# Performance work log

Measured on AMD Instinct MI355X. Metric: run time of the kernel, lower is better.

The kernel has to match this reference:

```python
import jax, jax.numpy as jnp
import numpy as np

N_EMBD = 384
HEAD_SIZE = 64
B, T = 512, 256


def setup_inputs() -> dict:
    key = jax.random.key(0)
    ks = jax.random.split(key, 7)
    s = 1.0 / np.sqrt(N_EMBD)  # torch Linear default init scale
    return {
        "x": jax.random.normal(ks[0], (B, T, N_EMBD), dtype=jnp.float32),
        "Wq": jax.random.uniform(ks[1], (N_EMBD, HEAD_SIZE), jnp.float32, -s, s),
        "bq": jax.random.uniform(ks[2], (HEAD_SIZE,), jnp.float32, -s, s),
        "Wk": jax.random.uniform(ks[3], (N_EMBD, HEAD_SIZE), jnp.float32, -s, s),
        "bk": jax.random.uniform(ks[4], (HEAD_SIZE,), jnp.float32, -s, s),
        "Wv": jax.random.uniform(ks[5], (N_EMBD, HEAD_SIZE), jnp.float32, -s, s),
        "bv": jax.random.uniform(ks[6], (HEAD_SIZE,), jnp.float32, -s, s),
    }


def reference(x, Wq, bq, Wk, bk, Wv, bv):
    # Single causal self-attention head (nanoGPT 'Head', eval mode: dropout = identity)
    q = x @ Wq + bq  # [B, T, H]
    k = x @ Wk + bk
    v = x @ Wv + bv
    Tq = x.shape[1]
    scale = x.shape[-1] ** -0.5  # NOTE: source scales by n_embd (C), not head_size
    wei = jnp.einsum("btd,bsd->bts", q, k) * scale  # [B, T, T]
    mask = jnp.tril(jnp.ones((Tq, Tq), dtype=bool))
    wei = jnp.where(mask, wei, -jnp.inf)
    wei = jax.nn.softmax(wei, axis=-1)
    return jnp.einsum("bts,bsd->btd", wei, v)  # [B, T, H]
```

## Files before the change

### kernel.cpp

```cpp
#include <hip/hip_runtime.h>
#include <hip/hip_bf16.h>


#define Bsz 512
#define Tt  256
#define Cc  384
#define Hh  64

typedef __attribute__((ext_vector_type(8))) short bf16x8;
typedef __attribute__((ext_vector_type(4))) float f32x4;

__device__ __forceinline__ unsigned short f2bf(float f) {
    unsigned int u = __float_as_uint(f);
    unsigned int r = (u + 0x7fffu + ((u >> 16) & 1u)) >> 16;
    return (unsigned short)r;
}
__device__ __forceinline__ float bf2f(unsigned short b) {
    return __uint_as_float(((unsigned int)b) << 16);
}
__device__ __forceinline__ bf16x8 pack8(float4 a, float4 b) {
    bf16x8 r;
    r[0] = (short)f2bf(a.x); r[1] = (short)f2bf(a.y);
    r[2] = (short)f2bf(a.z); r[3] = (short)f2bf(a.w);
    r[4] = (short)f2bf(b.x); r[5] = (short)f2bf(b.y);
    r[6] = (short)f2bf(b.z); r[7] = (short)f2bf(b.w);
    return r;
}

__global__ __launch_bounds__(256) void prep_kernel(const float* __restrict__ Wq,
                                                   const float* __restrict__ Wk,
                                                   const float* __restrict__ Wv,
                                                   unsigned short* __restrict__ wt) {
    int idx = blockIdx.x * 256 + threadIdx.x;
    if (idx >= 192 * 384) return;
    int n = idx / 384, k = idx - n * 384;
    const float* W = (n < 64) ? Wq : ((n < 128) ? Wk : Wv);
    wt[n * 384 + k] = f2bf(W[k * 64 + (n & 63)]);
}

__global__ __launch_bounds__(256, 2) void qkv_kernel(const float* __restrict__ x,
                                                     const float* __restrict__ bq,
                                                     const float* __restrict__ bk,
                                                     const float* __restrict__ bv,
                                                     const unsigned short* __restrict__ wt,
                                                     unsigned short* __restrict__ qws,
                                                     unsigned short* __restrict__ kws,
                                                     unsigned short* __restrict__ vws) {
    const int w = threadIdx.x >> 6;
    const int lane = threadIdx.x & 63;
    const int quad = lane >> 4;
    const int cl = lane & 15;
    const int rb = blockIdx.x * 128 + w * 32;

    f32x4 acc[2][12];
    for (int rt = 0; rt < 2; ++rt)
        for (int nt = 0; nt < 12; ++nt) acc[rt][nt] = (f32x4){0.f, 0.f, 0.f, 0.f};

    const float* xr0 = x + (size_t)(rb + cl) * Cc;
    const float* xr1 = x + (size_t)(rb + 16 + cl) * Cc;
    const unsigned short* wrow = wt + (size_t)cl * Cc + quad * 8;

    for (int ks = 0; ks < 12; ++ks) {
        const int k0 = ks * 32 + quad * 8;
        float4 xa = *(const float4*)(xr0 + k0);
        float4 xb = *(const float4*)(xr0 + k0 + 4);
        float4 xc = *(const float4*)(xr1 + k0);
        float4 xd = *(const float4*)(xr1 + k0 + 4);
        bf16x8 a0 = pack8(xa, xb);
        bf16x8 a1 = pack8(xc, xd);
#pragma unroll
        for (int nt = 0; nt < 12; ++nt) {
            bf16x8 bfr = *(const bf16x8*)(wrow + (size_t)nt * 16 * Cc + ks * 32);
            acc[0][nt] = __builtin_amdgcn_mfma_f32_16x16x32_bf16(a0, bfr, acc[0][nt], 0, 0, 0);
            acc[1][nt] = __builtin_amdgcn_mfma_f32_16x16x32_bf16(a1, bfr, acc[1][nt], 0, 0, 0);
        }
    }

    for (int nt = 0; nt < 12; ++nt) {
        int col = nt * 16 + cl;
        float bias = (col < 64) ? bq[col] : ((col < 128) ? bk[col - 64] : bv[col - 128]);
        unsigned short* wsout = (col < 64) ? qws : ((col < 128) ? kws : vws);
        int h = col & 63;
        for (int rt = 0; rt < 2; ++rt)
            for (int r = 0; r < 4; ++r) {
                int m = rb + rt * 16 + quad * 4 + r;
                wsout[(size_t)m * Hh + h] = f2bf(acc[rt][nt][r] + bias);
            }
    }
}

__global__ __launch_bounds__(256) void attn_kernel(const unsigned short* __restrict__ qws,
                                                   const unsigned short* __restrict__ kws,
                                                   const unsigned short* __restrict__ vws,
                                                   float* __restrict__ out) {
    __shared__ unsigned short Kl[128 * 72];
    __shared__ unsigned short Vt[64 * 136];
    __shared__ unsigned short Ql[64 * 72];
    __shared__ unsigned short Pl[4 * 16 * 136];

    const int w = threadIdx.x >> 6;
    const int lane = threadIdx.x & 63;
    const int quad = lane >> 4;
    const int cl = lane & 15;
    const int qbase = blockIdx.x * 64;
    const int bb = blockIdx.y;
    const int qrow0 = qbase + w * 16;
    const float SL2E = 0.07362224f;

    for (int l = threadIdx.x; l < 512; l += 256) {
        int row = l >> 3, off = (l & 7) << 3;
        uint4 v = *(const uint4*)(qws + ((size_t)(bb * Tt + qbase + row)) * Hh + off);
        *(uint4*)&Ql[row * 72 + off] = v;
    }

    f32x4 o[4];
    for (int ht = 0; ht < 4; ++ht) o[ht] = (f32x4){0.f, 0.f, 0.f, 0.f};
    float rs[4] = {0.f, 0.f, 0.f, 0.f};

    const int nchunk = (qbase + 191) >> 7;
    for (int c = 0; c < nchunk; ++c) {
        const int kbase = c * 128;
        for (int l = threadIdx.x; l < 1024; l += 256) {
            int row = l >> 3, off = (l & 7) << 3;
            uint4 v = *(const uint4*)(kws + ((size_t)(bb * Tt + kbase + row)) * Hh + off);
            *(uint4*)&Kl[row * 72 + off] = v;
        }
        for (int l = threadIdx.x; l < 1024; l += 256) {
            int s = l >> 3, h0 = (l & 7) << 3;
            uint4 v = *(const uint4*)(vws + ((size_t)(bb * Tt + kbase + s)) * Hh + h0);
            const unsigned short* e = (const unsigned short*)&v;
            for (int j = 0; j < 8; ++j) Vt[(h0 + j) * 136 + s] = e[j];
        }
        __syncthreads();

        bf16x8 aq0 = *(const bf16x8*)&Ql[(w * 16 + cl) * 72 + quad * 8];
        bf16x8 aq1 = *(const bf16x8*)&Ql[(w * 16 + cl) * 72 + 32 + quad * 8];

        const int qlast = qrow0 + 15;
        const int kt = min(8, ((qlast - kbase) >> 4) + 1);
        const int ktr = (kt + 1) & ~1;

        for (int ct = 0; ct < kt; ++ct) {
            f32x4 sc = (f32x4){0.f, 0.f, 0.f, 0.f};
            bf16x8 b0 = *(const bf16x8*)&Kl[(ct * 16 + cl) * 72 + quad * 8];
            bf16x8 b1 = *(const bf16x8*)&Kl[(ct * 16 + cl) * 72 + 32 + quad * 8];
            sc = __builtin_amdgcn_mfma_f32_16x16x32_bf16(aq0, b0, sc, 0, 0, 0);
            sc = __builtin_amdgcn_mfma_f32_16x16x32_bf16(aq1, b1, sc, 0, 0, 0);
            int key = kbase + ct * 16 + cl;
            for (int r = 0; r < 4; ++r) {
                int qg = qrow0 + quad * 4 + r;
                float p = 0.f;
                if (key <= qg) p = exp2f(sc[r] * SL2E);
                unsigned short pb = f2bf(p);
                rs[r] += bf2f(pb);
                Pl[(w * 16 + quad * 4 + r) * 136 + ct * 16 + cl] = pb;
            }
        }
        for (int ct = kt; ct < ktr; ++ct)
            for (int r = 0; r < 4; ++r)
                Pl[(w * 16 + quad * 4 + r) * 136 + ct * 16 + cl] = 0;

        asm volatile("s_waitcnt lgkmcnt(0)" ::: "memory");

        for (int ks2 = 0; ks2 < (ktr >> 1); ++ks2) {
            bf16x8 ap = *(const bf16x8*)&Pl[(w * 16 + cl) * 136 + ks2 * 32 + quad * 8];
            for (int ht = 0; ht < 4; ++ht) {
                bf16x8 bvf = *(const bf16x8*)&Vt[(ht * 16 + cl) * 136 + ks2 * 32 + quad * 8];
                o[ht] = __builtin_amdgcn_mfma_f32_16x16x32_bf16(ap, bvf, o[ht], 0, 0, 0);
            }
        }
        if (c + 1 < nchunk) __syncthreads();
    }

    for (int r = 0; r < 4; ++r) {
        float s = rs[r];
        s += __shfl_xor(s, 1);
        s += __shfl_xor(s, 2);
        s += __shfl_xor(s, 4);
        s += __shfl_xor(s, 8);
        float inv = 1.0f / s;
        int t = qrow0 + quad * 4 + r;
        for (int ht = 0; ht < 4; ++ht)
            out[((size_t)(bb * Tt + t)) * Hh + ht * 16 + cl] = o[ht][r] * inv;
    }
}

extern "C" void kernel_launch(void* const* d_in, const int* in_sizes, int n_in,
                              void* d_out, int out_size, void* d_ws, size_t ws_size,
                              hipStream_t stream) {
    const float* x  = (const float*)d_in[0];
    const float* Wq = (const float*)d_in[1];
    const float* bq = (const float*)d_in[2];
    const float* Wk = (const float*)d_in[3];
    const float* bk = (const float*)d_in[4];
    const float* Wv = (const float*)d_in[5];
    const float* bv = (const float*)d_in[6];
    float* out = (float*)d_out;

    char* ws = (char*)d_ws;
    unsigned short* wt  = (unsigned short*)(ws);
    unsigned short* qws = (unsigned short*)(ws + (size_t)(1  << 20));
    unsigned short* kws = (unsigned short*)(ws + (size_t)(17 << 20));
    unsigned short* vws = (unsigned short*)(ws + (size_t)(33 << 20));

    prep_kernel<<<288, 256, 0, stream>>>(Wq, Wk, Wv, wt);
    qkv_kernel<<<1024, 256, 0, stream>>>(x, bq, bk, bv, wt, qws, kws, vws);
    attn_kernel<<<dim3(4, Bsz), 256, 0, stream>>>(qws, kws, vws, out);
}
```

Measured before the change: 388.4 us.

## Split QKV GEMM across waves, prefetch operands, store V transposed globally

The QKV projection kernel now gives each wave 32 rows by 96 columns instead of 32 by 192, uses twice as many blocks, and raises the occupancy hint. It also software-prefetches the next k-step of x and weights into registers. V is written to global memory already transposed as [B,H,T] with packed 64-bit stores, so the attention kernel loads V into LDS with vector copies instead of a scalar transpose scatter. Other changes are a packed bf16 conversion helper and added unroll pragmas. The cost is more redundant reads of x across column groups and strided transposed global writes for V.

```diff
diff --git a/kernel.cpp b/kernel.cpp
--- a/kernel.cpp
+++ b/kernel.cpp
@@ -19,12 +19,12 @@
     return __uint_as_float(((unsigned int)b) << 16);
 }
 __device__ __forceinline__ bf16x8 pack8(float4 a, float4 b) {
-    bf16x8 r;
-    r[0] = (short)f2bf(a.x); r[1] = (short)f2bf(a.y);
-    r[2] = (short)f2bf(a.z); r[3] = (short)f2bf(a.w);
-    r[4] = (short)f2bf(b.x); r[5] = (short)f2bf(b.y);
-    r[6] = (short)f2bf(b.z); r[7] = (short)f2bf(b.w);
-    return r;
+    union { __hip_bfloat162 h2[4]; bf16x8 v; } u;
+    u.h2[0] = __float22bfloat162_rn(float2{a.x, a.y});
+    u.h2[1] = __float22bfloat162_rn(float2{a.z, a.w});
+    u.h2[2] = __float22bfloat162_rn(float2{b.x, b.y});
+    u.h2[3] = __float22bfloat162_rn(float2{b.z, b.w});
+    return u.v;
 }
 
 __global__ __launch_bounds__(256) void prep_kernel(const float* __restrict__ Wq,
@@ -38,60 +38,103 @@
     wt[n * 384 + k] = f2bf(W[k * 64 + (n & 63)]);
 }
 
-__global__ __launch_bounds__(256, 2) void qkv_kernel(const float* __restrict__ x,
+__global__ __launch_bounds__(256, 4) void qkv_kernel(const float* __restrict__ x,
                                                      const float* __restrict__ bq,
                                                      const float* __restrict__ bk,
                                                      const float* __restrict__ bv,
                                                      const unsigned short* __restrict__ wt,
                                                      unsigned short* __restrict__ qws,
                                                      unsigned short* __restrict__ kws,
-                                                     unsigned short* __restrict__ vws) {
+                                                     unsigned short* __restrict__ vtg) {
     const int w = threadIdx.x >> 6;
     const int lane = threadIdx.x & 63;
     const int quad = lane >> 4;
     const int cl = lane & 15;
-    const int rb = blockIdx.x * 128 + w * 32;
-
-    f32x4 acc[2][12];
+    const int rg = w >> 1, cg = w & 1;
+    const int rw = blockIdx.x * 64 + rg * 32;
+
+    f32x4 acc[2][6];
+#pragma unroll
     for (int rt = 0; rt < 2; ++rt)
-        for (int nt = 0; nt < 12; ++nt) acc[rt][nt] = (f32x4){0.f, 0.f, 0.f, 0.f};
-
-    const float* xr0 = x + (size_t)(rb + cl) * Cc;
-    const float* xr1 = x + (size_t)(rb + 16 + cl) * Cc;
-    const unsigned short* wrow = wt + (size_t)cl * Cc + quad * 8;
-
+#pragma unroll
+        for (int nt = 0; nt < 6; ++nt) acc[rt][nt] = (f32x4){0.f, 0.f, 0.f, 0.f};
+
+    const float* xr0 = x + (size_t)(rw + cl) * Cc + quad * 8;
+    const float* xr1 = x + (size_t)(rw + 16 + cl) * Cc + quad * 8;
+    const unsigned short* wrow = wt + ((size_t)(cg * 96) + cl) * Cc + quad * 8;
+
+    float4 cx[4];
+    bf16x8 cb[6];
+    cx[0] = *(const float4*)(xr0);
+    cx[1] = *(const float4*)(xr0 + 4);
+    cx[2] = *(const float4*)(xr1);
+    cx[3] = *(const float4*)(xr1 + 4);
+#pragma unroll
+    for (int nt = 0; nt < 6; ++nt) cb[nt] = *(const bf16x8*)(wrow + (size_t)nt * 16 * Cc);
+
+#pragma unroll
     for (int ks = 0; ks < 12; ++ks) {
-        const int k0 = ks * 32 + quad * 8;
-        float4 xa = *(const float4*)(xr0 + k0);
-        float4 xb = *(const float4*)(xr0 + k0 + 4);
-        float4 xc = *(const float4*)(xr1 + k0);
-        float4 xd = *(const float4*)(xr1 + k0 + 4);
-        bf16x8 a0 = pack8(xa, xb);
-        bf16x8 a1 = pack8(xc, xd);
-#pragma unroll
-        for (int nt = 0; nt < 12; ++nt) {
-            bf16x8 bfr = *(const bf16x8*)(wrow + (size_t)nt * 16 * Cc + ks * 32);
-            acc[0][nt] = __builtin_amdgcn_mfma_f32_16x16x32_bf16(a0, bfr, acc[0][nt], 0, 0, 0);
-            acc[1][nt] = __builtin_amdgcn_mfma_f32_16x16x32_bf16(a1, bfr, acc[1][nt], 0, 0, 0);
-        }
-    }
-
-    for (int nt = 0; nt < 12; ++nt) {
-        int col = nt * 16 + cl;
-        float bias = (col < 64) ? bq[col] : ((col < 128) ? bk[col - 64] : bv[col - 128]);
-        unsigned short* wsout = (col < 64) ? qws : ((col < 128) ? kws : vws);
-        int h = col & 63;
-        for (int rt = 0; rt < 2; ++rt)
-            for (int r = 0; r < 4; ++r) {
-                int m = rb + rt * 16 + quad * 4 + r;
-                wsout[(size_t)m * Hh + h] = f2bf(acc[rt][nt][r] + bias);
+        float4 nx[4];
+        bf16x8 nb[6];
+        if (ks + 1 < 12) {
+            const int k1 = (ks + 1) * 32;
+            nx[0] = *(const float4*)(xr0 + k1);
+            nx[1] = *(const float4*)(xr0 + k1 + 4);
+            nx[2] = *(const float4*)(xr1 + k1);
+            nx[3] = *(const float4*)(xr1 + k1 + 4);
+#pragma unroll
+            for (int nt = 0; nt < 6; ++nt)
+                nb[nt] = *(const bf16x8*)(wrow + (size_t)nt * 16 * Cc + k1);
+        }
+        bf16x8 a0 = pack8(cx[0], cx[1]);
+        bf16x8 a1 = pack8(cx[2], cx[3]);
+#pragma unroll
+        for (int nt = 0; nt < 6; ++nt) {
+            acc[0][nt] = __builtin_amdgcn_mfma_f32_16x16x32_bf16(a0, cb[nt], acc[0][nt], 0, 0, 0);
+            acc[1][nt] = __builtin_amdgcn_mfma_f32_16x16x32_bf16(a1, cb[nt], acc[1][nt], 0, 0, 0);
+        }
+        if (ks + 1 < 12) {
+#pragma unroll
+            for (int i = 0; i < 4; ++i) cx[i] = nx[i];
+#pragma unroll
+            for (int nt = 0; nt < 6; ++nt) cb[nt] = nb[nt];
+        }
+    }
+
+#pragma unroll
+    for (int nt = 0; nt < 6; ++nt) {
+        int col = cg * 96 + nt * 16 + cl;
+        if (col < 128) {
+            float bias = (col < 64) ? bq[col] : bk[col - 64];
+            unsigned short* o = (col < 64) ? qws : kws;
+            int h = col & 63;
+#pragma unroll
+            for (int rt = 0; rt < 2; ++rt)
+#pragma unroll
+                for (int r = 0; r < 4; ++r) {
+                    int m = rw + rt * 16 + quad * 4 + r;
+                    o[(size_t)m * Hh + h] = f2bf(acc[rt][nt][r] + bias);
+                }
+        } else {
+            int h = col - 128;
+            float bias = bv[h];
+#pragma unroll
+            for (int rt = 0; rt < 2; ++rt) {
+                int m0 = rw + rt * 16 + quad * 4;
+                unsigned long long pk =
+                      (unsigned long long)f2bf(acc[rt][nt][0] + bias)
+                    | ((unsigned long long)f2bf(acc[rt][nt][1] + bias) << 16)
+                    | ((unsigned long long)f2bf(acc[rt][nt][2] + bias) << 32)
+                    | ((unsigned long long)f2bf(acc[rt][nt][3] + bias) << 48);
+                *(unsigned long long*)&vtg[((size_t)(m0 >> 8) * Hh + h) * Tt + (m0 & 255)] = pk;
             }
+        }
     }
 }
 
 __global__ __launch_bounds__(256) void attn_kernel(const unsigned short* __restrict__ qws,
                                                    const unsigned short* __restrict__ kws,
-                                                   const unsigned short* __restrict__ vws,
+                                                   const unsigned short* __restrict__ vtg,
                                                    float* __restrict__ out) {
     __shared__ unsigned short Kl[128 * 72];
     __shared__ unsigned short Vt[64 * 136];
@@ -114,6 +157,7 @@
     }
 
     f32x4 o[4];
+#pragma unroll
     for (int ht = 0; ht < 4; ++ht) o[ht] = (f32x4){0.f, 0.f, 0.f, 0.f};
     float rs[4] = {0.f, 0.f, 0.f, 0.f};
 
@@ -126,10 +170,9 @@
             *(uint4*)&Kl[row * 72 + off] = v;
         }
         for (int l = threadIdx.x; l < 1024; l += 256) {
-            int s = l >> 3, h0 = (l & 7) << 3;
-            uint4 v = *(const uint4*)(vws + ((size_t)(bb * Tt + kbase + s)) * Hh + h0);
-            const unsigned short* e = (const unsigned short*)&v;
-            for (int j = 0; j < 8; ++j) Vt[(h0 + j) * 136 + s] = e[j];
+            int h = l >> 4, off = (l & 15) << 3;
+            uint4 v = *(const uint4*)(vtg + ((size_t)(bb * Hh + h)) * Tt + kbase + off);
+            *(uint4*)&Vt[h * 136 + off] = v;
         }
         __syncthreads();
 
@@ -147,6 +190,7 @@
             sc = __builtin_amdgcn_mfma_f32_16x16x32_bf16(aq0, b0, sc, 0, 0, 0);
             sc = __builtin_amdgcn_mfma_f32_16x16x32_bf16(aq1, b1, sc, 0, 0, 0);
             int key = kbase + ct * 16 + cl;
+#pragma unroll
             for (int r = 0; r < 4; ++r) {
                 int qg = qrow0 + quad * 4 + r;
                 float p = 0.f;
@@ -157,6 +201,7 @@
             }
         }
         for (int ct = kt; ct < ktr; ++ct)
+#pragma unroll
             for (int r = 0; r < 4; ++r)
                 Pl[(w * 16 + quad * 4 + r) * 136 + ct * 16 + cl] = 0;
 
@@ -164,6 +209,7 @@
 
         for (int ks2 = 0; ks2 < (ktr >> 1); ++ks2) {
             bf16x8 ap = *(const bf16x8*)&Pl[(w * 16 + cl) * 136 + ks2 * 32 + quad * 8];
+#pragma unroll
             for (int ht = 0; ht < 4; ++ht) {
                 bf16x8 bvf = *(const bf16x8*)&Vt[(ht * 16 + cl) * 136 + ks2 * 32 + quad * 8];
                 o[ht] = __builtin_amdgcn_mfma_f32_16x16x32_bf16(ap, bvf, o[ht], 0, 0, 0);
@@ -172,6 +218,7 @@
         if (c + 1 < nchunk) __syncthreads();
     }
 
+#pragma unroll
     for (int r = 0; r < 4; ++r) {
         float s = rs[r];
         s += __shfl_xor(s, 1);
@@ -180,6 +227,7 @@
         s += __shfl_xor(s, 8);
         float inv = 1.0f / s;
         int t = qrow0 + quad * 4 + r;
+#pragma unroll
         for (int ht = 0; ht < 4; ++ht)
             out[((size_t)(bb * Tt + t)) * Hh + ht * 16 + cl] = o[ht][r] * inv;
     }
@@ -201,9 +249,9 @@
     unsigned short* wt  = (unsigned short*)(ws);
     unsigned short* qws = (unsigned short*)(ws + (size_t)(1  << 20));
     unsigned short* kws = (unsigned short*)(ws + (size_t)(17 << 20));
-    unsigned short* vws = (unsigned short*)(ws + (size_t)(33 << 20));
+    unsigned short* vtg = (unsigned short*)(ws + (size_t)(33 << 20));
 
     prep_kernel<<<288, 256, 0, stream>>>(Wq, Wk, Wv, wt);
-    qkv_kernel<<<1024, 256, 0, stream>>>(x, bq, bk, bv, wt, qws, kws, vws);
-    attn_kernel<<<dim3(4, Bsz), 256, 0, stream>>>(qws, kws, vws, out);
-}
+    qkv_kernel<<<2048, 256, 0, stream>>>(x, bq, bk, bv, wt, qws, kws, vtg);
+    attn_kernel<<<dim3(4, Bsz), 256, 0, stream>>>(qws, kws, vtg, out);
+}
```

New measurement: 401.1 us. 1.03x slower.
